# Performance work log

Measured on AMD Instinct MI355X. Metric: run time of the kernel, lower is better.

## Reference

```python
import jax, jax.numpy as jnp
import numpy as np

# ---- static config (mirrors PaCoVoxelLoss init) ----
NUM_QUERIES = 20
FACTOR = 64
NUM_GT = 12
K_NEIGHBORS = 8          # repulsion.num_neighbors
REP_EPS = 1e-12          # repulsion.epsilon
BANDWIDTH = 0.03         # repulsion.kernel_bandwidth
RADIUS = 0.07            # repulsion.radius
ALPHA_PARAM = 0.5
BETA_CHAMFER = 20.0
W_CLS, W_REP, W_CH1, W_CH2 = 1.0, 1.0, 1.0, 1.0
PAD_COST = 1e6           # pad value to square the rectangular assignment problem


def _hungarian(cost):
    # Jonker-Volgenant / e-maxx shortest augmenting path; cost: (n, n) float64.
    # Returns col_to_row: for each column j, the row assigned to it.
    n = cost.shape[0]
    INF = 1e18
    u = np.zeros(n + 1); v = np.zeros(n + 1)
    p = np.zeros(n + 1, dtype=np.int64)
    way = np.zeros(n + 1, dtype=np.int64)
    for i in range(1, n + 1):
        p[0] = i; j0 = 0
        minv = np.full(n + 1, INF)
        used = np.zeros(n + 1, dtype=bool)
        while True:
            used[j0] = True
            i0 = p[j0]; delta = INF; j1 = 0
            for j in range(1, n + 1):
                if not used[j]:
                    cur = cost[i0 - 1, j - 1] - u[i0] - v[j]
                    if cur < minv[j]:
                        minv[j] = cur; way[j] = j0
                    if minv[j] < delta:
                        delta = minv[j]; j1 = j
            for j in range(n + 1):
                if used[j]:
                    u[p[j]] += delta; v[j] -= delta
                else:
                    minv[j] -= delta
            j0 = j1
            if p[j0] == 0:
                break
        while j0 != 0:
            j1 = way[j0]; p[j0] = p[j1]; j0 = j1
    return p[1:] - 1


def _match(cost_np):
    # cost_np: (B, Q, P) with P <= Q -> rows (B, P): pred row matched to each gt col.
    Bn, Qn, Pn = cost_np.shape
    rows = np.zeros((Bn, Pn), dtype=np.int64)
    for b in range(Bn):
        sq = np.full((Qn, Qn), PAD_COST, dtype=np.float64)
        sq[:, :Pn] = cost_np[b].astype(np.float64)
        rows[b] = _hungarian(sq)[:Pn]
    return rows


def _gather_q(A, rows):
    # A: (B, Q, P), rows: (B, P) -> A[b, rows[b,p], p] : (B, P)
    return jnp.take_along_axis(A, rows[:, None, :], axis=1)[:, 0, :]


def _bce_logits(x, t):
    return jnp.maximum(x, 0.0) - x * t + jnp.log1p(jnp.exp(-jnp.abs(x)))


def _cost_terms(pred_normals, pred_distances, gt_normals, gt_distances, points, gt_masks):
    mask_f = gt_masks.astype(points.dtype)           # (B, P, N)
    cnt = mask_f.sum(-1)                             # (B, P)
    # |points . n_q - d_q| for all query planes: (B, Q, N)
    pp = jnp.abs(jnp.einsum('bnd,bqd->bqn', points, pred_normals) - pred_distances[:, :, None])
    cham_raw = jnp.einsum('bqn,bpn->bqp', pp, mask_f) / jnp.maximum(cnt, 1.0)[:, None, :]
    has = (cnt > 0)[:, None, :]                      # (B, 1, P)
    normal_sim = 1.0 - jnp.abs(jnp.einsum('bqd,bpd->bqp', pred_normals, gt_normals))
    dist_diff = jnp.abs(pred_distances[:, :, None] - gt_distances[:, None, :])
    cost = normal_sim + 0.5 * dist_diff + 5.0 * jnp.where(has, cham_raw, 1.0)
    return cost, cham_raw, normal_sim, dist_diff, has


def _losses(pred_logits, pred_normals, pred_distances, gt_normals, gt_distances,
            points, reconstructed_points, gt, gt_masks, rows):
    _, cham_raw, normal_sim, dist_diff, has = _cost_terms(
        pred_normals, pred_distances, gt_normals, gt_distances, points, gt_masks)

    # classification loss: target 1 at matched pred rows
    Qn = pred_logits.shape[1]
    cls_target = jax.nn.one_hot(rows, Qn, dtype=pred_logits.dtype).sum(axis=1)  # (B, Q)
    cls_loss = _bce_logits(pred_logits, cls_target).mean()

    # param loss over matched pairs (mean over P matches, mean over B)
    param_loss = (_gather_q(normal_sim, rows).mean(-1) + _gather_q(dist_diff, rows).mean(-1)).mean()

    # pvd chamfer: point-to-plane term, zero for empty masks, /P /B
    pvd_chamfer = _gather_q(jnp.where(has, cham_raw, 0.0), rows).mean()

    # repulsion loss on per-query point groups
    Bn = reconstructed_points.shape[0]
    rp = reconstructed_points.reshape(Bn, NUM_QUERIES, FACTOR, 3)
    d2 = jnp.sum((rp[:, :, :, None, :] - rp[:, :, None, :, :]) ** 2, axis=-1)  # (B,Q,F,F)
    _, idx = jax.lax.top_k(-d2, K_NEIGHBORS)       # k nearest incl. self
    dn = jnp.maximum(jnp.take_along_axis(d2, idx[..., 1:], axis=-1), REP_EPS)  # (B,Q,F,k-1)
    w = jnp.exp(-dn / BANDWIDTH ** 2)
    rep = jnp.maximum(jnp.mean((RADIUS - jnp.sqrt(dn)) * w, axis=(2, 3)), 0.0).mean()

    # fine-grained chamfer (L1 and L2) between reconstructed and gt clouds
    diff = reconstructed_points[:, :, None, :] - gt[:, None, :, :]  # (B, M, G, 3)
    d1 = jnp.abs(diff).sum(-1)
    d2c = (diff ** 2).sum(-1)
    ch1 = (0.5 * (d1.min(axis=2).mean(axis=1) + d1.min(axis=1).mean(axis=1))).mean()
    ch2 = (0.5 * (d2c.min(axis=2).mean(axis=1) + d2c.min(axis=1).mean(axis=1))).mean()

    total = (W_CLS * cls_loss + ALPHA_PARAM * param_loss + BETA_CHAMFER * pvd_chamfer
             + W_REP * rep + W_CH1 * ch1 + W_CH2 * ch2)
    return total


def setup_inputs() -> dict:
    key = jax.random.key(0)
    ks = jax.random.split(key, 10)
    B, Q, P, N, G = 8, NUM_QUERIES, NUM_GT, 4096, 2048

    def unit(k, shape):
        v = jax.random.normal(k, shape, dtype=jnp.float32)
        return v / jnp.linalg.norm(v, axis=-1, keepdims=True)

    return {
        'pred_logits': jax.random.normal(ks[0], (B, Q), dtype=jnp.float32),
        'pred_normals': unit(ks[1], (B, Q, 3)),
        'pred_distances': jax.random.normal(ks[2], (B, Q), dtype=jnp.float32),
        'gt_normals': unit(ks[3], (B, P, 3)),
        'gt_distances': jax.random.normal(ks[4], (B, P), dtype=jnp.float32),
        'gt_masks': jax.random.bernoulli(ks[5], 0.3, (B, P, N)),
        'points': jax.random.normal(ks[6], (B, N, 3), dtype=jnp.float32),
        'reconstructed_points': 0.5 * jax.random.normal(ks[7], (B, Q * FACTOR, 3), dtype=jnp.float32),
        'gt': jax.random.normal(ks[8], (B, G, 3), dtype=jnp.float32),
        'gt_index': jax.random.randint(ks[9], (B, G), 0, P, dtype=jnp.int64) if jax.config.jax_enable_x64 else jax.random.randint(ks[9], (B, G), 0, P, dtype=jnp.int32),
    }


def reference(pred_logits, pred_normals, pred_distances, gt_normals, gt_distances,
              points, reconstructed_points, gt, gt_masks, gt_index):
    cost = _cost_terms(pred_normals, pred_distances, gt_normals, gt_distances, points, gt_masks)[0]
    rows = jnp.asarray(_match(np.asarray(cost)))  # Hungarian (host, like scipy in original)
    return _losses(pred_logits, pred_normals, pred_distances, gt_normals, gt_distances,
                   points, reconstructed_points, gt, gt_masks, rows)
```

## Files before the change

kernel.cpp:

```cpp
#include <hip/hip_runtime.h>
#include <math.h>

#define Bn 8
#define Qn 20
#define Pn 12
#define Nn 4096
#define Gn 2048
#define Mn 1280
#define Fn 64
#define KNB 7
#define NCOST 160
#define NREP 20
#define NCHA 40
#define NCHB 64
#define NBLK 284
#define C2_TARGET 113
#define SCOPE_AGENT __HIP_MEMORY_SCOPE_AGENT


__device__ __forceinline__ float aread(float* p) { return atomicAdd(p, 0.0f); }
__device__ __forceinline__ void ast(float* p, float v) {
    __hip_atomic_store(p, v, __ATOMIC_RELAXED, SCOPE_AGENT);
}
__device__ __forceinline__ float ald(const float* p) {
    return __hip_atomic_load(p, __ATOMIC_RELAXED, SCOPE_AGENT);
}

__device__ __forceinline__ int rdlane_i(int v, int l) {
    return __builtin_amdgcn_readlane(v, l);
}
__device__ __forceinline__ float rdlane_f(float v, int l) {
    return __int_as_float(__builtin_amdgcn_readlane(__float_as_int(v), l));
}
__device__ __forceinline__ unsigned wave_min_u32(unsigned x) {
    unsigned t;
    t = (unsigned)__builtin_amdgcn_update_dpp((int)0xFFFFFFFF, (int)x, 0x111, 0xF, 0xF, false);
    x = t < x ? t : x;
    t = (unsigned)__builtin_amdgcn_update_dpp((int)0xFFFFFFFF, (int)x, 0x112, 0xF, 0xF, false);
    x = t < x ? t : x;
    t = (unsigned)__builtin_amdgcn_update_dpp((int)0xFFFFFFFF, (int)x, 0x114, 0xF, 0xF, false);
    x = t < x ? t : x;
    t = (unsigned)__builtin_amdgcn_update_dpp((int)0xFFFFFFFF, (int)x, 0x118, 0xF, 0xF, false);
    x = t < x ? t : x;
    t = (unsigned)__builtin_amdgcn_update_dpp((int)0xFFFFFFFF, (int)x, 0x142, 0xF, 0xF, false);
    x = t < x ? t : x;
    t = (unsigned)__builtin_amdgcn_update_dpp((int)0xFFFFFFFF, (int)x, 0x143, 0xF, 0xF, false);
    x = t < x ? t : x;
    return x;
}

__device__ __forceinline__ void wait_zero(float* ws, unsigned init) {
    unsigned* z = (unsigned*)(ws + 7785);
    while (__hip_atomic_load(z, __ATOMIC_ACQUIRE, SCOPE_AGENT) - init != 1u)
        __builtin_amdgcn_s_sleep(1);
}

__device__ __forceinline__ void bump_c2(float* ws, float* out, unsigned init) {
    unsigned* c2P = (unsigned*)(ws + 7784);
    unsigned old = __hip_atomic_fetch_add(c2P, 1u, __ATOMIC_ACQ_REL, SCOPE_AGENT);
    if (old - init == (unsigned)(C2_TARGET - 1)) {
        float* acc = ws + 7776;
        float a0 = aread(&acc[0]);
        float a1 = aread(&acc[1]);
        float a2 = aread(&acc[2]);
        float a3 = aread(&acc[3]);
        float a4 = aread(&acc[4]);
        float a5 = aread(&acc[5]);
        out[0] = a0 + 0.5f * a1 + 20.f * a2 + a3 + a4 + a5;
        unsigned* w = (unsigned*)ws;
        __hip_atomic_store(&w[7784], init, __ATOMIC_RELAXED, SCOPE_AGENT);
        __hip_atomic_store(&w[7785], init, __ATOMIC_RELAXED, SCOPE_AGENT);
        __hip_atomic_store(&w[7786], init, __ATOMIC_RELAXED, SCOPE_AGENT);
        for (int k = 0; k < 8; ++k)
            __hip_atomic_store(&w[7788 + k], init, __ATOMIC_RELAXED, SCOPE_AGENT);
    }
}

__global__ __launch_bounds__(512, 2)
void fused_kernel(const float* __restrict__ pred_logits,
                  const float* __restrict__ pred_normals,
                  const float* __restrict__ pred_distances,
                  const float* __restrict__ gt_normals,
                  const float* __restrict__ gt_distances,
                  const float* __restrict__ points,
                  const int*   __restrict__ gt_masks,
                  const float* __restrict__ recon,
                  const float* __restrict__ gt,
                  float* __restrict__ ws,
                  float* __restrict__ out) {
    __shared__ __align__(16) float smem[8192];
    __shared__ int sflag;
    const int blk = blockIdx.x;
    const int tid = threadIdx.x;

    float* cham = ws;
    float* ns   = ws + 1920;
    float* dd   = ws + 3840;
    float* cost = ws + 5760;
    float* cnt  = ws + 7680;
    float* acc  = ws + 7776;
    unsigned* baseP = (unsigned*)(ws + 7783);
    unsigned* repcP = (unsigned*)(ws + 7786);
    unsigned* doneB = (unsigned*)(ws + 7788);
    float* rep_part = ws + 7808;

    const unsigned init = __hip_atomic_load(baseP, __ATOMIC_RELAXED, SCOPE_AGENT);

    if (blk < NCOST) {
        if (blk == 0 && tid < 6) ast(&acc[tid], 0.f);
        const int b = blk / Qn, q = blk % Qn;
        const float nx = pred_normals[(b * Qn + q) * 3 + 0];
        const float ny = pred_normals[(b * Qn + q) * 3 + 1];
        const float nz = pred_normals[(b * Qn + q) * 3 + 2];
        const float dq = pred_distances[b * Qn + q];

        if (tid < 256) {
            float accs[Pn], accw[Pn];
#pragma unroll
            for (int p = 0; p < Pn; ++p) { accs[p] = 0.f; accw[p] = 0.f; }
            const float* ptb = points + (size_t)b * Nn * 3;
            const int*   mb  = gt_masks + (size_t)b * Pn * Nn;
            for (int n = tid; n < Nn; n += 256) {
                float px = ptb[n * 3 + 0], py = ptb[n * 3 + 1], pz = ptb[n * 3 + 2];
                float pp = fabsf(px * nx + py * ny + pz * nz - dq);
#pragma unroll
                for (int p = 0; p < Pn; ++p) {
                    float m = (float)mb[(size_t)p * Nn + n];
                    accs[p] += pp * m;
                    accw[p] += m;
                }
            }
#pragma unroll
            for (int p = 0; p < Pn; ++p) {
                smem[p * 256 + tid] = accs[p];
                smem[(p + Pn) * 256 + tid] = accw[p];
            }
        }
        __syncthreads();
        for (int off = 128; off > 0; off >>= 1) {
            if (tid < off) {
#pragma unroll
                for (int r = 0; r < 2 * Pn; ++r) smem[r * 256 + tid] += smem[r * 256 + tid + off];
            }
            __syncthreads();
        }
        if (tid < Pn) {
            const int p = tid;
            float c  = smem[(p + Pn) * 256];
            float cv = smem[p * 256] / fmaxf(c, 1.f);
            float gnx = gt_normals[(b * Pn + p) * 3 + 0];
            float gny = gt_normals[(b * Pn + p) * 3 + 1];
            float gnz = gt_normals[(b * Pn + p) * 3 + 2];
            float nsim = 1.f - fabsf(nx * gnx + ny * gny + nz * gnz);
            float ddv  = fabsf(dq - gt_distances[b * Pn + p]);
            int idx = (b * Qn + q) * Pn + p;
            ast(&cham[idx], cv);
            ast(&ns[idx],   nsim);
            ast(&dd[idx],   ddv);
            ast(&cost[idx], nsim + 0.5f * ddv + 5.f * ((c > 0.f) ? cv : 1.f));
            if (q == 0) ast(&cnt[b * Pn + p], c);
        }
        __syncthreads();
        if (tid == 0) {
            if (blk == 0) {
                unsigned* z = (unsigned*)(ws + 7785);
                __hip_atomic_store(z, init + 1u, __ATOMIC_RELEASE, SCOPE_AGENT);
            }
            __hip_atomic_fetch_add(&doneB[b], 1u, __ATOMIC_RELEASE, SCOPE_AGENT);
        }
        if (blk >= 8) return;

        if (tid == 0) {
            while (__hip_atomic_load(&doneB[blk], __ATOMIC_RELAXED, SCOPE_AGENT) - init != 20u)
                __builtin_amdgcn_s_sleep(2);
            (void)__hip_atomic_load(&doneB[blk], __ATOMIC_ACQUIRE, SCOPE_AGENT);
        }
        __syncthreads();

        if (tid < 64) {
            const int b2 = blk;
            const int t = tid;
            const int col = t;
            const bool isCol = (col >= 1 && col <= Qn);

            float cr[Pn];
#pragma unroll
            for (int k = 0; k < Pn; ++k) cr[k] = 0.f;
            if (isCol) {
                const float* cb = cost + ((size_t)b2 * Qn + (col - 1)) * Pn;
#pragma unroll
                for (int k = 0; k < Pn; ++k) cr[k] = ald(&cb[k]);
            }

            float v = 0.f, u = 0.f, minv = 0.f;
            int way = 0, p = 0;

            for (int i = 1; i <= Pn; ++i) {
                minv = 1e30f;
                bool used = false;
                bool rowInPath = false;
                int j0s = 0;
                while (true) {
                    if (col == j0s) used = true;
                    int i0s = (j0s == 0) ? i : rdlane_i(p, j0s);
                    if (t == i0s) rowInPath = true;
                    float u_i0 = rdlane_f(u, i0s);
                    const int bs = i0s - 1;
                    float l10 = (bs & 1) ? cr[1]  : cr[0];
                    float l11 = (bs & 1) ? cr[3]  : cr[2];
                    float l12 = (bs & 1) ? cr[5]  : cr[4];
                    float l13 = (bs & 1) ? cr[7]  : cr[6];
                    float l14 = (bs & 1) ? cr[9]  : cr[8];
                    float l15 = (bs & 1) ? cr[11] : cr[10];
                    float l20 = (bs & 2) ? l11 : l10;
                    float l21 = (bs & 2) ? l13 : l12;
                    float l22 = (bs & 2) ? l15 : l14;
                    float cij = (bs >= 8) ? l22 : ((bs >= 4) ? l21 : l20);
                    if (isCol && !used) {
                        float cur = cij - u_i0 - v;
                        if (cur < minv) { minv = cur; way = j0s; }
                    }
                    float mv = (isCol && !used) ? minv : 1e30f;
                    unsigned kb = __float_as_uint(mv);
                    kb = ((int)kb < 0) ? ~kb : (kb | 0x80000000u);
                    kb = (kb & ~31u) | (unsigned)(col & 31);
                    unsigned kmin = (unsigned)rdlane_i((int)wave_min_u32(kb), 63);
                    int j1 = (int)(kmin & 31u);
                    float delta = rdlane_f(minv, j1);
                    if (used || col == 0) v -= delta;
                    else if (isCol)       minv -= delta;
                    if (rowInPath)        u += delta;
                    j0s = j1;
                    int pj0 = rdlane_i(p, j0s);
                    if (pj0 == 0) break;
                }
                while (j0s != 0) {
                    int wj = rdlane_i(way, j0s);
                    int pw = (wj == 0) ? i : rdlane_i(p, wj);
                    if (col == j0s) p = pw;
                    j0s = wj;
                }
            }

            float cls = 0.f, par = 0.f, pvd = 0.f;
            if (isCol) {
                float x = pred_logits[b2 * Qn + (col - 1)];
                float tgt = (p > 0) ? 1.f : 0.f;
                cls = fmaxf(x, 0.f) - x * tgt + log1pf(expf(-fabsf(x)));
                if (p > 0) {
                    int idx = (b2 * Qn + (col - 1)) * Pn + (p - 1);
                    par = ald(&ns[idx]) + ald(&dd[idx]);
                    pvd = (ald(&cnt[b2 * Pn + (p - 1)]) > 0.f) ? ald(&cham[idx]) : 0.f;
                }
            }
            for (int off = 32; off > 0; off >>= 1) {
                cls += __shfl_down(cls, off);
                par += __shfl_down(par, off);
                pvd += __shfl_down(pvd, off);
            }
            if (t == 0) {
                wait_zero(ws, init);
                atomicAdd(&acc[0], cls / (float)(Bn * Qn));
                atomicAdd(&acc[1], par / (float)(Bn * Pn));
                atomicAdd(&acc[2], pvd / (float)(Bn * Pn));
                bump_c2(ws, out, init);
            }
        }
        return;
    } else if (blk < NCOST + NREP) {
        const int wave = tid >> 6, lane = tid & 63;
        const int g = (blk - NCOST) * 8 + wave;
        float* xs = smem + wave * 192;
        float* ys = xs + 64;
        float* zs = xs + 128;
        const float* base = recon + (size_t)g * Fn * 3;
        xs[lane] = base[lane * 3 + 0];
        ys[lane] = base[lane * 3 + 1];
        zs[lane] = base[lane * 3 + 2];
        float best[KNB];
#pragma unroll
        for (int k = 0; k < KNB; ++k) best[k] = 3.4e38f;
        const float xi = xs[lane], yi = ys[lane], zi = zs[lane];
        for (int j = 0; j < Fn; ++j) {
            float dx = xi - xs[j], dy = yi - ys[j], dz = zi - zs[j];
            float d2 = dx * dx + dy * dy + dz * dz;
            d2 = (j == lane) ? 3.4e38f : d2;
#pragma unroll
            for (int k = 0; k < KNB; ++k) {
                float lo = fminf(best[k], d2);
                float hi = fmaxf(best[k], d2);
                best[k] = lo;
                d2 = hi;
            }
        }
        float sum = 0.f;
#pragma unroll
        for (int k = 0; k < KNB; ++k) {
            float dn = fmaxf(best[k], 1e-12f);
            float w  = expf(-dn / (0.03f * 0.03f));
            sum += (0.07f - sqrtf(dn)) * w;
        }
        for (int off = 32; off > 0; off >>= 1) sum += __shfl_down(sum, off);
        if (lane == 0) ast(&rep_part[g], fmaxf(sum / (float)(Fn * KNB), 0.f));
        __syncthreads();
        if (tid == 0) {
            unsigned old = __hip_atomic_fetch_add(repcP, 1u, __ATOMIC_ACQ_REL, SCOPE_AGENT);
            sflag = (old - init == (unsigned)(NREP - 1)) ? 1 : 0;
        }
        __syncthreads();
        if (sflag) {
            float* s1 = smem + 2048;
            if (tid < 256)
                s1[tid] = (tid < Bn * Qn) ? ald(&rep_part[tid]) / (float)(Bn * Qn) : 0.f;
            __syncthreads();
            for (int off = 128; off > 0; off >>= 1) {
                if (tid < off) s1[tid] += s1[tid + off];
                __syncthreads();
            }
            if (tid == 0) {
                wait_zero(ws, init);
                atomicAdd(&acc[3], s1[0]);
                bump_c2(ws, out, init);
            }
        }
        return;
    }

    {
        const int a = blk - (NCOST + NREP);
        const bool isA = (a < NCHA);
        const int chunk = isA ? a : (a - NCHA);
        const int lt = tid & 255;
        const int half = tid >> 8;
        const int idx = chunk * 256 + lt;
        const float* inner;
        const float* op;
        int ninner;
        float scale;
        if (isA) {
            const int b = idx / Mn;
            inner = gt + (size_t)b * Gn * 3;
            op = recon + (size_t)idx * 3;
            ninner = Gn;
            scale = 0.5f / (float)(Bn * Mn);
        } else {
            const int b = idx / Gn;
            inner = recon + (size_t)b * Mn * 3;
            op = gt + (size_t)idx * 3;
            ninner = Mn;
            scale = 0.5f / (float)(Bn * Gn);
        }
        float4* tile = reinterpret_cast<float4*>(smem);
        for (int j = tid; j < ninner; j += 512) {
            const float* ip = inner + j * 3;
            float4 tv;
            tv.x = ip[0]; tv.y = ip[1]; tv.z = ip[2]; tv.w = 0.f;
            tile[j] = tv;
        }
        __syncthreads();
        const float x = op[0], y = op[1], z = op[2];
        const int j0 = half * (ninner >> 1), j1 = j0 + (ninner >> 1);
        float m1 = 3.4e38f, m2 = 3.4e38f;
#pragma unroll 4
        for (int j = j0; j < j1; ++j) {
            float4 tv = tile[j];
            float dx = x - tv.x, dy = y - tv.y, dz = z - tv.z;
            float d1 = fabsf(dx) + fabsf(dy) + fabsf(dz);
            float d2 = dx * dx + dy * dy + dz * dz;
            m1 = fminf(m1, d1); m2 = fminf(m2, d2);
        }
        __syncthreads();
        float* s1 = smem;
        float* s2 = smem + 512;
        s1[tid] = m1;
        s2[tid] = m2;
        __syncthreads();
        float* t1 = smem + 1024;
        float* t2 = smem + 1280;
        if (tid < 256) {
            float M1 = fminf(s1[tid], s1[tid + 256]);
            float M2 = fminf(s2[tid], s2[tid + 256]);
            t1[tid] = M1 * scale;
            t2[tid] = M2 * scale;
        }
        __syncthreads();
        for (int off = 128; off > 0; off >>= 1) {
            if (tid < off) { t1[tid] += t1[tid + off]; t2[tid] += t2[tid + off]; }
            __syncthreads();
        }
        if (tid == 0) {
            wait_zero(ws, init);
            atomicAdd(&acc[4], t1[0]);
            atomicAdd(&acc[5], t2[0]);
            bump_c2(ws, out, init);
        }
    }
}

extern "C" void kernel_launch(void* const* d_in, const int* in_sizes, int n_in,
                              void* d_out, int out_size, void* d_ws, size_t ws_size,
                              hipStream_t stream) {
    const float* pred_logits    = (const float*)d_in[0];
    const float* pred_normals   = (const float*)d_in[1];
    const float* pred_distances = (const float*)d_in[2];
    const float* gt_normals     = (const float*)d_in[3];
    const float* gt_distances   = (const float*)d_in[4];
    const int*   gt_masks       = (const int*)d_in[5];
    const float* points         = (const float*)d_in[6];
    const float* recon          = (const float*)d_in[7];
    const float* gt             = (const float*)d_in[8];

    fused_kernel<<<NBLK, 512, 0, stream>>>(pred_logits, pred_normals, pred_distances,
                                           gt_normals, gt_distances, points, gt_masks,
                                           recon, gt, (float*)d_ws, (float*)d_out);
}
```

Baseline: 114.1 us.

## Replace atomic accumulators with per-block partial slots and reorder block roles

Removes the shared atomicAdd accumulators and the wait-for-zero spin. Each producer block now stores its partials to its own padded slot, and the last finisher sums them. Cost-block indexing is interleaved across batches and the repulsion blocks move to the end of the grid, with chamfer chunks also interleaved. Per-batch done counters sit on separate cache lines to cut contention. The intent is to drop serialization on hot atomic addresses and the initialization dependency, at the cost of a longer final gather.

After: 110.0 us. -3.5%, faster.

```diff
diff --git a/kernel.cpp b/kernel.cpp
--- a/kernel.cpp
+++ b/kernel.cpp
@@ -10,15 +10,14 @@
 #define Fn 64
 #define KNB 7
 #define NCOST 160
-#define NREP 20
 #define NCHA 40
 #define NCHB 64
+#define NREP 20
 #define NBLK 284
 #define C2_TARGET 113
 #define SCOPE_AGENT __HIP_MEMORY_SCOPE_AGENT
 
 
-__device__ __forceinline__ float aread(float* p) { return atomicAdd(p, 0.0f); }
 __device__ __forceinline__ void ast(float* p, float v) {
     __hip_atomic_store(p, v, __ATOMIC_RELAXED, SCOPE_AGENT);
 }
@@ -49,30 +48,35 @@
     return x;
 }
 
-__device__ __forceinline__ void wait_zero(float* ws, unsigned init) {
-    unsigned* z = (unsigned*)(ws + 7785);
-    while (__hip_atomic_load(z, __ATOMIC_ACQUIRE, SCOPE_AGENT) - init != 1u)
-        __builtin_amdgcn_s_sleep(1);
-}
-
 __device__ __forceinline__ void bump_c2(float* ws, float* out, unsigned init) {
-    unsigned* c2P = (unsigned*)(ws + 7784);
+    unsigned* c2P = (unsigned*)(ws + 7936);
     unsigned old = __hip_atomic_fetch_add(c2P, 1u, __ATOMIC_ACQ_REL, SCOPE_AGENT);
     if (old - init == (unsigned)(C2_TARGET - 1)) {
-        float* acc = ws + 7776;
-        float a0 = aread(&acc[0]);
-        float a1 = aread(&acc[1]);
-        float a2 = aread(&acc[2]);
-        float a3 = aread(&acc[3]);
-        float a4 = aread(&acc[4]);
-        float a5 = aread(&acc[5]);
+        float a0 = 0.f, a1 = 0.f, a2 = 0.f, a4 = 0.f, a5 = 0.f;
+#pragma unroll
+        for (int b = 0; b < 8; ++b) {
+            a0 += ald(ws + 8000 + 16 * b + 0);
+            a1 += ald(ws + 8000 + 16 * b + 1);
+            a2 += ald(ws + 8000 + 16 * b + 2);
+        }
+#pragma unroll
+        for (int c = 0; c < NCHA; ++c) {
+            a4 += ald(ws + 8192 + 16 * c + 0);
+            a5 += ald(ws + 8192 + 16 * c + 1);
+        }
+#pragma unroll
+        for (int c = 0; c < NCHB; ++c) {
+            a4 += ald(ws + 8896 + 16 * c + 0);
+            a5 += ald(ws + 8896 + 16 * c + 1);
+        }
+        float a3 = ald(ws + 7952);
         out[0] = a0 + 0.5f * a1 + 20.f * a2 + a3 + a4 + a5;
         unsigned* w = (unsigned*)ws;
-        __hip_atomic_store(&w[7784], init, __ATOMIC_RELAXED, SCOPE_AGENT);
-        __hip_atomic_store(&w[7785], init, __ATOMIC_RELAXED, SCOPE_AGENT);
-        __hip_atomic_store(&w[7786], init, __ATOMIC_RELAXED, SCOPE_AGENT);
-        for (int k = 0; k < 8; ++k)
-            __hip_atomic_store(&w[7788 + k], init, __ATOMIC_RELAXED, SCOPE_AGENT);
+        __hip_atomic_store(&w[7936], init, __ATOMIC_RELAXED, SCOPE_AGENT);
+        __hip_atomic_store(&w[7968], init, __ATOMIC_RELAXED, SCOPE_AGENT);
+#pragma unroll
+        for (int b = 0; b < 8; ++b)
+            __hip_atomic_store(&w[7808 + 16 * b], init, __ATOMIC_RELAXED, SCOPE_AGENT);
     }
 }
 
@@ -98,17 +102,14 @@
     float* dd   = ws + 3840;
     float* cost = ws + 5760;
     float* cnt  = ws + 7680;
-    float* acc  = ws + 7776;
     unsigned* baseP = (unsigned*)(ws + 7783);
-    unsigned* repcP = (unsigned*)(ws + 7786);
-    unsigned* doneB = (unsigned*)(ws + 7788);
-    float* rep_part = ws + 7808;
+    unsigned* repcP = (unsigned*)(ws + 7968);
+    float* rep_part = ws + 10240;
 
     const unsigned init = __hip_atomic_load(baseP, __ATOMIC_RELAXED, SCOPE_AGENT);
 
     if (blk < NCOST) {
-        if (blk == 0 && tid < 6) ast(&acc[tid], 0.f);
-        const int b = blk / Qn, q = blk % Qn;
+        const int b = blk & 7, q = blk >> 3;
         const float nx = pred_normals[(b * Qn + q) * 3 + 0];
         const float ny = pred_normals[(b * Qn + q) * 3 + 1];
         const float nz = pred_normals[(b * Qn + q) * 3 + 2];
@@ -161,19 +162,16 @@
             if (q == 0) ast(&cnt[b * Pn + p], c);
         }
         __syncthreads();
+        if (tid == 0)
+            __hip_atomic_fetch_add((unsigned*)(ws + 7808 + 16 * b), 1u,
+                                   __ATOMIC_RELEASE, SCOPE_AGENT);
+        if (blk >= 8) return;
+
         if (tid == 0) {
-            if (blk == 0) {
-                unsigned* z = (unsigned*)(ws + 7785);
-                __hip_atomic_store(z, init + 1u, __ATOMIC_RELEASE, SCOPE_AGENT);
-            }
-            __hip_atomic_fetch_add(&doneB[b], 1u, __ATOMIC_RELEASE, SCOPE_AGENT);
-        }
-        if (blk >= 8) return;
-
-        if (tid == 0) {
-            while (__hip_atomic_load(&doneB[blk], __ATOMIC_RELAXED, SCOPE_AGENT) - init != 20u)
+            unsigned* dB = (unsigned*)(ws + 7808 + 16 * blk);
+            while (__hip_atomic_load(dB, __ATOMIC_RELAXED, SCOPE_AGENT) - init != 20u)
                 __builtin_amdgcn_s_sleep(2);
-            (void)__hip_atomic_load(&doneB[blk], __ATOMIC_ACQUIRE, SCOPE_AGENT);
+            (void)__hip_atomic_load(dB, __ATOMIC_ACQUIRE, SCOPE_AGENT);
         }
         __syncthreads();
 
@@ -259,77 +257,20 @@
                 pvd += __shfl_down(pvd, off);
             }
             if (t == 0) {
-                wait_zero(ws, init);
-                atomicAdd(&acc[0], cls / (float)(Bn * Qn));
-                atomicAdd(&acc[1], par / (float)(Bn * Pn));
-                atomicAdd(&acc[2], pvd / (float)(Bn * Pn));
+                float* slot = ws + 8000 + 16 * b2;
+                ast(slot + 0, cls / (float)(Bn * Qn));
+                ast(slot + 1, par / (float)(Bn * Pn));
+                ast(slot + 2, pvd / (float)(Bn * Pn));
                 bump_c2(ws, out, init);
             }
         }
         return;
-    } else if (blk < NCOST + NREP) {
-        const int wave = tid >> 6, lane = tid & 63;
-        const int g = (blk - NCOST) * 8 + wave;
-        float* xs = smem + wave * 192;
-        float* ys = xs + 64;
-        float* zs = xs + 128;
-        const float* base = recon + (size_t)g * Fn * 3;
-        xs[lane] = base[lane * 3 + 0];
-        ys[lane] = base[lane * 3 + 1];
-        zs[lane] = base[lane * 3 + 2];
-        float best[KNB];
-#pragma unroll
-        for (int k = 0; k < KNB; ++k) best[k] = 3.4e38f;
-        const float xi = xs[lane], yi = ys[lane], zi = zs[lane];
-        for (int j = 0; j < Fn; ++j) {
-            float dx = xi - xs[j], dy = yi - ys[j], dz = zi - zs[j];
-            float d2 = dx * dx + dy * dy + dz * dz;
-            d2 = (j == lane) ? 3.4e38f : d2;
-#pragma unroll
-            for (int k = 0; k < KNB; ++k) {
-                float lo = fminf(best[k], d2);
-                float hi = fmaxf(best[k], d2);
-                best[k] = lo;
-                d2 = hi;
-            }
-        }
-        float sum = 0.f;
-#pragma unroll
-        for (int k = 0; k < KNB; ++k) {
-            float dn = fmaxf(best[k], 1e-12f);
-            float w  = expf(-dn / (0.03f * 0.03f));
-            sum += (0.07f - sqrtf(dn)) * w;
-        }
-        for (int off = 32; off > 0; off >>= 1) sum += __shfl_down(sum, off);
-        if (lane == 0) ast(&rep_part[g], fmaxf(sum / (float)(Fn * KNB), 0.f));
-        __syncthreads();
-        if (tid == 0) {
-            unsigned old = __hip_atomic_fetch_add(repcP, 1u, __ATOMIC_ACQ_REL, SCOPE_AGENT);
-            sflag = (old - init == (unsigned)(NREP - 1)) ? 1 : 0;
-        }
-        __syncthreads();
-        if (sflag) {
-            float* s1 = smem + 2048;
-            if (tid < 256)
-                s1[tid] = (tid < Bn * Qn) ? ald(&rep_part[tid]) / (float)(Bn * Qn) : 0.f;
-            __syncthreads();
-            for (int off = 128; off > 0; off >>= 1) {
-                if (tid < off) s1[tid] += s1[tid + off];
-                __syncthreads();
-            }
-            if (tid == 0) {
-                wait_zero(ws, init);
-                atomicAdd(&acc[3], s1[0]);
-                bump_c2(ws, out, init);
-            }
-        }
-        return;
-    }
-
-    {
-        const int a = blk - (NCOST + NREP);
+    } else if (blk < NCOST + NCHA + NCHB) {
+        const int a = blk - NCOST;
         const bool isA = (a < NCHA);
-        const int chunk = isA ? a : (a - NCHA);
+        int chunk;
+        if (isA) { int r = a;         chunk = (r & 7) * 5 + (r >> 3); }
+        else     { int r = a - NCHA;  chunk = (r & 7) * 8 + (r >> 3); }
         const int lt = tid & 255;
         const int half = tid >> 8;
         const int idx = chunk * 256 + lt;
@@ -337,18 +278,21 @@
         const float* op;
         int ninner;
         float scale;
+        float* slot;
         if (isA) {
             const int b = idx / Mn;
             inner = gt + (size_t)b * Gn * 3;
             op = recon + (size_t)idx * 3;
             ninner = Gn;
             scale = 0.5f / (float)(Bn * Mn);
+            slot = ws + 8192 + 16 * chunk;
         } else {
             const int b = idx / Gn;
             inner = recon + (size_t)b * Mn * 3;
             op = gt + (size_t)idx * 3;
             ninner = Mn;
             scale = 0.5f / (float)(Bn * Gn);
+            slot = ws + 8896 + 16 * chunk;
         }
         float4* tile = reinterpret_cast<float4*>(smem);
         for (int j = tid; j < ninner; j += 512) {
@@ -389,10 +333,67 @@
             __syncthreads();
         }
         if (tid == 0) {
-            wait_zero(ws, init);
-            atomicAdd(&acc[4], t1[0]);
-            atomicAdd(&acc[5], t2[0]);
+            ast(slot + 0, t1[0]);
+            ast(slot + 1, t2[0]);
             bump_c2(ws, out, init);
+        }
+        return;
+    }
+
+    {
+        const int wave = tid >> 6, lane = tid & 63;
+        const int g = (blk - (NCOST + NCHA + NCHB)) * 8 + wave;
+        float* xs = smem + wave * 192;
+        float* ys = xs + 64;
+        float* zs = xs + 128;
+        const float* base = recon + (size_t)g * Fn * 3;
+        xs[lane] = base[lane * 3 + 0];
+        ys[lane] = base[lane * 3 + 1];
+        zs[lane] = base[lane * 3 + 2];
+        float best[KNB];
+#pragma unroll
+        for (int k = 0; k < KNB; ++k) best[k] = 3.4e38f;
+        const float xi = xs[lane], yi = ys[lane], zi = zs[lane];
+        for (int j = 0; j < Fn; ++j) {
+            float dx = xi - xs[j], dy = yi - ys[j], dz = zi - zs[j];
+            float d2 = dx * dx + dy * dy + dz * dz;
+            d2 = (j == lane) ? 3.4e38f : d2;
+#pragma unroll
+            for (int k = 0; k < KNB; ++k) {
+                float lo = fminf(best[k], d2);
+                float hi = fmaxf(best[k], d2);
+                best[k] = lo;
+                d2 = hi;
+            }
+        }
+        float sum = 0.f;
+#pragma unroll
+        for (int k = 0; k < KNB; ++k) {
+            float dn = fmaxf(best[k], 1e-12f);
+            float w  = expf(-dn / (0.03f * 0.03f));
+            sum += (0.07f - sqrtf(dn)) * w;
+        }
+        for (int off = 32; off > 0; off >>= 1) sum += __shfl_down(sum, off);
+        if (lane == 0) ast(&rep_part[g], fmaxf(sum / (float)(Fn * KNB), 0.f));
+        __syncthreads();
+        if (tid == 0) {
+            unsigned old = __hip_atomic_fetch_add(repcP, 1u, __ATOMIC_ACQ_REL, SCOPE_AGENT);
+            sflag = (old - init == (unsigned)(NREP - 1)) ? 1 : 0;
+        }
+        __syncthreads();
+        if (sflag) {
+            float* s1 = smem + 2048;
+            if (tid < 256)
+                s1[tid] = (tid < Bn * Qn) ? ald(&rep_part[tid]) / (float)(Bn * Qn) : 0.f;
+            __syncthreads();
+            for (int off = 128; off > 0; off >>= 1) {
+                if (tid < off) s1[tid] += s1[tid + off];
+                __syncthreads();
+            }
+            if (tid == 0) {
+                ast(ws + 7952, s1[0]);
+                bump_c2(ws, out, init);
+            }
         }
     }
 }
```
